# Optimization experiments

Hardware: AMD Instinct MI355X
Metric: run time of the kernel (lower is better)

The kernel has to match this reference:

```python
import jax, jax.numpy as jnp
import numpy as np

EPS = 1e-5

def _act_quant(x):
    # per-token int8 absmax quantization (BitNet b1.58)
    scale = 127.0 / jnp.clip(jnp.max(jnp.abs(x), axis=-1, keepdims=True), EPS)
    return jnp.clip(jnp.round(x * scale), -128.0, 127.0) / scale

def _weight_quant(w):
    # per-tensor ternary quantization: round(w/mean|w|) clipped to {-1,0,1}
    scale = 1.0 / jnp.clip(jnp.mean(jnp.abs(w)), EPS)
    return jnp.clip(jnp.round(w * scale), -1.0, 1.0) / scale

def _ste(x, q):
    # straight-through estimator: forward uses q, backward passes through x
    return x + jax.lax.stop_gradient(q - x)

def bitlinear(x, w):
    xq = _ste(x, _act_quant(x))
    wq = _ste(w, _weight_quant(w))
    return jnp.einsum('btd,hd->bth', xq, wq)

def setup_inputs() -> dict:
    key = jax.random.key(0)
    k1, k2, k3 = jax.random.split(key, 3)
    B, T, D, H = 4, 1024, 2048, 8192
    x = jax.random.normal(k1, (B, T, D), dtype=jnp.float32)
    w1 = jax.random.normal(k2, (H, D), dtype=jnp.float32) * 0.02
    w2 = jax.random.normal(k3, (D, H), dtype=jnp.float32) * 0.02
    return {"x": x, "w1": w1, "w2": w2}

def reference(x, w1, w2):
    h = jax.nn.relu(bitlinear(x, w1))   # [B, T, H]
    out = bitlinear(h, w2)              # [B, T, D]
    return out
```

## Files before the change

### kernel.cpp

```cpp
#include <hip/hip_runtime.h>
#include <hip/hip_bf16.h>

#define EPSF 1e-5f

typedef int v4i __attribute__((ext_vector_type(4)));
typedef short v8s __attribute__((ext_vector_type(8)));

static constexpr int BB = 4, TT = 1024, DD = 2048, HH = 8192;
static constexpr int MROWS = BB * TT;
static constexpr long long WCOUNT = (long long)DD * HH;


__device__ __forceinline__ void async_copy16(const void* g, void* l) {
  __builtin_amdgcn_global_load_lds(
      (const __attribute__((address_space(1))) unsigned int*)g,
      (__attribute__((address_space(3))) unsigned int*)l,
      16, 0, 0);
}

__device__ __forceinline__ int pack4(float a, float b, float c, float d,
                                     float scale, float lo, float hi) {
  int ia = (int)fminf(fmaxf(rintf(a * scale), lo), hi);
  int ib = (int)fminf(fmaxf(rintf(b * scale), lo), hi);
  int ic = (int)fminf(fmaxf(rintf(c * scale), lo), hi);
  int id = (int)fminf(fmaxf(rintf(d * scale), lo), hi);
  return (ia & 0xff) | ((ib & 0xff) << 8) | ((ic & 0xff) << 16) | ((id & 0xff) << 24);
}

__device__ __forceinline__ float abs4(float4 v) {
  return fmaxf(fmaxf(fabsf(v.x), fabsf(v.y)), fmaxf(fabsf(v.z), fabsf(v.w)));
}

__device__ __forceinline__ int blockMaxI256(int v) {
  #pragma unroll
  for (int off = 32; off; off >>= 1) v = max(v, __shfl_down(v, off, 64));
  __shared__ int sm[4];
  int lane = threadIdx.x & 63, wv = threadIdx.x >> 6;
  if (lane == 0) sm[wv] = v;
  __syncthreads();
  return max(max(sm[0], sm[1]), max(sm[2], sm[3]));
}

__device__ __forceinline__ void swizzle_tiles(int& mt, int& nt) {
  int Mt = gridDim.y, Nt = gridDim.x;
  int id = blockIdx.y * Nt + blockIdx.x;
  int c = id & 7, k = id >> 3;
  int pm = (Mt >= Nt) ? 4 : 2;
  int PM = Mt / pm, PN = Nt / (8 / pm);
  int pr = c % pm, pc = c / pm;
  mt = pr * PM + (k % PM);
  nt = pc * PN + (k / PM);
}


__global__ __launch_bounds__(256) void abs_sum_kernel(
    const float* __restrict__ w1, const float* __restrict__ w2,
    float* __restrict__ partials) {
  const int y = blockIdx.y, bid = blockIdx.x, t = threadIdx.x;
  const int lane = t & 63, wv = t >> 6;
  const float4* w4 = (const float4*)(y ? w2 : w1);
  const long long base = (long long)bid * 2048;
  float4 u[8];
  #pragma unroll
  for (int k = 0; k < 8; k++) u[k] = w4[base + t + k * 256];
  float s = 0.f;
  #pragma unroll
  for (int k = 0; k < 8; k++)
    s += fabsf(u[k].x) + fabsf(u[k].y) + fabsf(u[k].z) + fabsf(u[k].w);
  #pragma unroll
  for (int off = 32; off; off >>= 1) s += __shfl_down(s, off, 64);
  __shared__ float sm[4];
  if (lane == 0) sm[wv] = s;
  __syncthreads();
  if (t == 0) partials[y * 2048 + bid] = sm[0] + sm[1] + sm[2] + sm[3];
}


__global__ __launch_bounds__(256) void quant_w_kernel(
    const float* __restrict__ w1, const float* __restrict__ w2,
    const float* __restrict__ partials, float* __restrict__ meanw,
    signed char* __restrict__ q1, signed char* __restrict__ q2) {
  const int y = blockIdx.y, bid = blockIdx.x, t = threadIdx.x;
  const int lane = t & 63, wv = t >> 6;

  double d = 0.0;
  #pragma unroll
  for (int j = 0; j < 8; j++) d += (double)partials[y * 2048 + t + j * 256];
  #pragma unroll
  for (int off = 32; off; off >>= 1) d += __shfl_down(d, off, 64);
  __shared__ double smd[4];
  if (lane == 0) smd[wv] = d;
  __syncthreads();
  double sum = smd[0] + smd[1] + smd[2] + smd[3];
  float mean = fmaxf((float)(sum * (1.0 / (double)WCOUNT)), EPSF);
  if (bid == 0 && t == 0) meanw[y] = mean;
  float sc = 1.0f / mean;

  const float4* w4 = (const float4*)(y ? w2 : w1);
  int* q4 = (int*)(y ? q2 : q1);
  const long long base = (long long)bid * 2048;
  float4 u[8];
  #pragma unroll
  for (int k = 0; k < 8; k++) u[k] = w4[base + t + k * 256];
  #pragma unroll
  for (int k = 0; k < 8; k++)
    q4[base + t + k * 256] = pack4(u[k].x, u[k].y, u[k].z, u[k].w, sc, -1.f, 1.f);
}


__global__ __launch_bounds__(256) void quant_x_kernel(
    const float* __restrict__ x, signed char* __restrict__ xq,
    float* __restrict__ ascale) {
  int lane = threadIdx.x & 63, wv = threadIdx.x >> 6;
  int row = blockIdx.x * 4 + wv;
  const float4* xr = (const float4*)(x + (size_t)row * DD);
  float4 v[8];
  #pragma unroll
  for (int j = 0; j < 8; j++) v[j] = xr[lane + j * 64];
  float m = 0.f;
  #pragma unroll
  for (int j = 0; j < 8; j++) m = fmaxf(m, abs4(v[j]));
  #pragma unroll
  for (int off = 32; off; off >>= 1) m = fmaxf(m, __shfl_down(m, off, 64));
  m = __shfl(m, 0, 64);
  float am = fmaxf(m, EPSF);
  float scale = 127.0f / am;
  int* out = (int*)(xq + (size_t)row * DD);
  #pragma unroll
  for (int j = 0; j < 8; j++)
    out[lane + j * 64] = pack4(v[j].x, v[j].y, v[j].z, v[j].w, scale, -128.f, 127.f);
  if (lane == 0) ascale[row] = am / 127.0f;
}


__global__ __launch_bounds__(256) void quant_h_kernel(
    const short* __restrict__ h, signed char* __restrict__ hq,
    float* __restrict__ a2, const float* __restrict__ a1,
    const float* __restrict__ meanw) {
  int row = blockIdx.x;
  int t = threadIdx.x;
  const v8s* hr = (const v8s*)(h + (size_t)row * HH);
  v8s v[4];
  #pragma unroll
  for (int i = 0; i < 4; i++) v[i] = hr[t + i * 256];
  int mx = 0;
  #pragma unroll
  for (int i = 0; i < 4; i++)
    #pragma unroll
    for (int j = 0; j < 8; j++) mx = max(mx, (int)v[i][j]);
  int bmx = blockMaxI256(mx);
  float f = a1[row] * meanw[0];
  float maxh = (float)bmx * f;
  float am = fmaxf(maxh, EPSF);
  float scale = 127.0f / am;
  int* out = (int*)(hq + (size_t)row * HH);
  #pragma unroll
  for (int i = 0; i < 4; i++) {
    out[(t + i * 256) * 2] =
        pack4((float)v[i][0] * f, (float)v[i][1] * f, (float)v[i][2] * f,
              (float)v[i][3] * f, scale, -128.f, 127.f);
    out[(t + i * 256) * 2 + 1] =
        pack4((float)v[i][4] * f, (float)v[i][5] * f, (float)v[i][6] * f,
              (float)v[i][7] * f, scale, -128.f, 127.f);
  }
  if (t == 0) a2[row] = am / 127.0f;
}


template <int MODE, int BK>
__global__ __launch_bounds__(256) void gemm_i8_kernel(
    const signed char* __restrict__ A, const signed char* __restrict__ B,
    void* __restrict__ Cout, const float* __restrict__ ascale,
    const float* __restrict__ wmean_p, int M, int N, int K) {
  constexpr int CH = BK / 16;
  constexpr int SEGROWS = 1024 / BK;
  constexpr int SPW = BK / 32;
  __shared__ signed char As[128 * BK];
  __shared__ signed char Bs[128 * BK];

  const int t = threadIdx.x;
  const int lane = t & 63, wv = t >> 6;
  const int wm = wv >> 1, wn = wv & 1;
  int mt, nt;
  swizzle_tiles(mt, nt);
  const int m0 = mt * 128, n0 = nt * 128;
  const int q = lane >> 4;

  const signed char* aSrc[SPW];
  const signed char* bSrc[SPW];
  #pragma unroll
  for (int i = 0; i < SPW; i++) {
    int seg = wv * SPW + i;
    int r = seg * SEGROWS + lane / CH;
    int c = (lane % CH) ^ (r & (CH - 1));
    aSrc[i] = A + (size_t)(m0 + r) * K + c * 16;
    bSrc[i] = B + (size_t)(n0 + r) * K + c * 16;
  }

  v4i acc[4][4];
  #pragma unroll
  for (int i = 0; i < 4; i++)
    #pragma unroll
    for (int j = 0; j < 4; j++) {
      v4i z = {0, 0, 0, 0};
      acc[i][j] = z;
    }

  int rowA[4], rowB[4];
  #pragma unroll
  for (int i = 0; i < 4; i++) {
    rowA[i] = wm * 64 + i * 16 + (lane & 15);
    rowB[i] = wn * 64 + i * 16 + (lane & 15);
  }

  for (int k0 = 0; k0 < K; k0 += BK) {
    #pragma unroll
    for (int i = 0; i < SPW; i++) {
      async_copy16(aSrc[i] + k0, &As[(wv * SPW + i) * 1024]);
      async_copy16(bSrc[i] + k0, &Bs[(wv * SPW + i) * 1024]);
    }
    __syncthreads();
    #pragma unroll
    for (int kc = 0; kc < CH / 4; kc++) {
      v4i af[4], bf[4];
      #pragma unroll
      for (int i = 0; i < 4; i++) {
        int ca = (kc * 4 + q) ^ (rowA[i] & (CH - 1));
        af[i] = *(const v4i*)(As + rowA[i] * BK + ca * 16);
        int cb = (kc * 4 + q) ^ (rowB[i] & (CH - 1));
        bf[i] = *(const v4i*)(Bs + rowB[i] * BK + cb * 16);
      }
      #pragma unroll
      for (int i = 0; i < 4; i++)
        #pragma unroll
        for (int j = 0; j < 4; j++)
          acc[i][j] = __builtin_amdgcn_mfma_i32_16x16x64_i8(af[i], bf[j], acc[i][j], 0, 0, 0);
    }
    __syncthreads();
  }

  if constexpr (MODE == 1) {
    short* C = (short*)Cout;
    #pragma unroll
    for (int i = 0; i < 4; i++) {
      int mBase = m0 + wm * 64 + i * 16 + q * 4;
      #pragma unroll
      for (int e = 0; e < 4; e++) {
        #pragma unroll
        for (int j = 0; j < 4; j++) {
          int n = n0 + wn * 64 + j * 16 + (lane & 15);
          int r = acc[i][j][e];
          r = r < 0 ? 0 : (r > 32767 ? 32767 : r);
          C[(size_t)(mBase + e) * N + n] = (short)r;
        }
      }
    }
  } else {
    float* C = (float*)Cout;
    float wmean = wmean_p[0];
    #pragma unroll
    for (int i = 0; i < 4; i++) {
      int mBase = m0 + wm * 64 + i * 16 + q * 4;
      #pragma unroll
      for (int e = 0; e < 4; e++) {
        float f = ascale[mBase + e] * wmean;
        #pragma unroll
        for (int j = 0; j < 4; j++) {
          int n = n0 + wn * 64 + j * 16 + (lane & 15);
          C[(size_t)(mBase + e) * N + n] = (float)acc[i][j][e] * f;
        }
      }
    }
  }
}


extern "C" void kernel_launch(void* const* d_in, const int* in_sizes, int n_in,
                              void* d_out, int out_size, void* d_ws, size_t ws_size,
                              hipStream_t stream) {
  const float* x  = (const float*)d_in[0];
  const float* w1 = (const float*)d_in[1];
  const float* w2 = (const float*)d_in[2];
  float* out = (float*)d_out;

  char* ws = (char*)d_ws;
  float* meanw = (float*)ws;
  float* partials = (float*)(ws + 1024);
  float* a1 = (float*)(ws + 20480);
  float* a2 = (float*)(ws + 40960);
  signed char* w1q = (signed char*)(ws + 65536);
  signed char* w2q = w1q + (size_t)WCOUNT;
  signed char* xq  = w2q + (size_t)WCOUNT;
  signed char* hq  = xq + (size_t)MROWS * DD;
  short* h16 = (short*)(hq + (size_t)MROWS * HH);

  abs_sum_kernel<<<dim3(2048, 2), 256, 0, stream>>>(w1, w2, partials);
  quant_w_kernel<<<dim3(2048, 2), 256, 0, stream>>>(w1, w2, partials, meanw, w1q, w2q);
  quant_x_kernel<<<MROWS / 4, 256, 0, stream>>>(x, xq, a1);
  gemm_i8_kernel<1, 128><<<dim3(HH / 128, MROWS / 128), 256, 0, stream>>>(
      xq, w1q, h16, nullptr, meanw, MROWS, HH, DD);
  quant_h_kernel<<<MROWS, 256, 0, stream>>>(h16, hq, a2, a1, meanw);
  gemm_i8_kernel<0, 256><<<dim3(DD / 128, MROWS / 128), 256, 0, stream>>>(
      hq, w2q, out, a2, &meanw[1], MROWS, DD, HH);
}
```

Baseline: 375.2 us.

## Use 32x32x32 int8 MFMA, fuse x-quant into abs-sum, widen h stores

The GEMM moves from a 4x4 grid of 16x16x64 int8 MFMAs per wave to a 2x2 grid of 32x32x32 MFMAs, which halves the LDS fragment loads per k-step and changes the epilogue row mapping. The x-quantization and weight abs-sum kernels are merged into one launch, saving a kernel launch and letting both run concurrently. quant_h now writes 8 bytes per store instead of two 4-byte stores. The larger MFMA changes the LDS access pattern against the existing swizzle and may cause bank conflicts or different instruction throughput.

```diff
diff --git a/kernel.cpp b/kernel.cpp
--- a/kernel.cpp
+++ b/kernel.cpp
@@ -4,6 +4,7 @@
 #define EPSF 1e-5f
 
 typedef int v4i __attribute__((ext_vector_type(4)));
+typedef int v16i __attribute__((ext_vector_type(16)));
 typedef short v8s __attribute__((ext_vector_type(8)));
 
 static constexpr int BB = 4, TT = 1024, DD = 2048, HH = 8192;
@@ -53,26 +54,50 @@
 }
 
 
-__global__ __launch_bounds__(256) void abs_sum_kernel(
+__global__ __launch_bounds__(256) void prep_kernel(
     const float* __restrict__ w1, const float* __restrict__ w2,
-    float* __restrict__ partials) {
-  const int y = blockIdx.y, bid = blockIdx.x, t = threadIdx.x;
+    const float* __restrict__ x, float* __restrict__ partials,
+    signed char* __restrict__ xq, float* __restrict__ ascale) {
+  __shared__ float sm[4];
+  const int bid = blockIdx.x, t = threadIdx.x;
   const int lane = t & 63, wv = t >> 6;
-  const float4* w4 = (const float4*)(y ? w2 : w1);
-  const long long base = (long long)bid * 2048;
-  float4 u[8];
-  #pragma unroll
-  for (int k = 0; k < 8; k++) u[k] = w4[base + t + k * 256];
-  float s = 0.f;
-  #pragma unroll
-  for (int k = 0; k < 8; k++)
-    s += fabsf(u[k].x) + fabsf(u[k].y) + fabsf(u[k].z) + fabsf(u[k].w);
-  #pragma unroll
-  for (int off = 32; off; off >>= 1) s += __shfl_down(s, off, 64);
-  __shared__ float sm[4];
-  if (lane == 0) sm[wv] = s;
-  __syncthreads();
-  if (t == 0) partials[y * 2048 + bid] = sm[0] + sm[1] + sm[2] + sm[3];
+
+  if (bid < 4096) {
+    const int y = bid >> 11, b = bid & 2047;
+    const float4* w4 = (const float4*)(y ? w2 : w1);
+    const long long base = (long long)b * 2048;
+    float4 u[8];
+    #pragma unroll
+    for (int k = 0; k < 8; k++) u[k] = w4[base + t + k * 256];
+    float s = 0.f;
+    #pragma unroll
+    for (int k = 0; k < 8; k++)
+      s += fabsf(u[k].x) + fabsf(u[k].y) + fabsf(u[k].z) + fabsf(u[k].w);
+    #pragma unroll
+    for (int off = 32; off; off >>= 1) s += __shfl_down(s, off, 64);
+    if (lane == 0) sm[wv] = s;
+    __syncthreads();
+    if (t == 0) partials[y * 2048 + b] = sm[0] + sm[1] + sm[2] + sm[3];
+  } else {
+    int row = (bid - 4096) * 4 + wv;
+    const float4* xr = (const float4*)(x + (size_t)row * DD);
+    float4 v[8];
+    #pragma unroll
+    for (int j = 0; j < 8; j++) v[j] = xr[lane + j * 64];
+    float m = 0.f;
+    #pragma unroll
+    for (int j = 0; j < 8; j++) m = fmaxf(m, abs4(v[j]));
+    #pragma unroll
+    for (int off = 32; off; off >>= 1) m = fmaxf(m, __shfl_down(m, off, 64));
+    m = __shfl(m, 0, 64);
+    float am = fmaxf(m, EPSF);
+    float scale = 127.0f / am;
+    int* out = (int*)(xq + (size_t)row * DD);
+    #pragma unroll
+    for (int j = 0; j < 8; j++)
+      out[lane + j * 64] = pack4(v[j].x, v[j].y, v[j].z, v[j].w, scale, -128.f, 127.f);
+    if (lane == 0) ascale[row] = am / 127.0f;
+  }
 }
 
 
@@ -108,31 +133,6 @@
 }
 
 
-__global__ __launch_bounds__(256) void quant_x_kernel(
-    const float* __restrict__ x, signed char* __restrict__ xq,
-    float* __restrict__ ascale) {
-  int lane = threadIdx.x & 63, wv = threadIdx.x >> 6;
-  int row = blockIdx.x * 4 + wv;
-  const float4* xr = (const float4*)(x + (size_t)row * DD);
-  float4 v[8];
-  #pragma unroll
-  for (int j = 0; j < 8; j++) v[j] = xr[lane + j * 64];
-  float m = 0.f;
-  #pragma unroll
-  for (int j = 0; j < 8; j++) m = fmaxf(m, abs4(v[j]));
-  #pragma unroll
-  for (int off = 32; off; off >>= 1) m = fmaxf(m, __shfl_down(m, off, 64));
-  m = __shfl(m, 0, 64);
-  float am = fmaxf(m, EPSF);
-  float scale = 127.0f / am;
-  int* out = (int*)(xq + (size_t)row * DD);
-  #pragma unroll
-  for (int j = 0; j < 8; j++)
-    out[lane + j * 64] = pack4(v[j].x, v[j].y, v[j].z, v[j].w, scale, -128.f, 127.f);
-  if (lane == 0) ascale[row] = am / 127.0f;
-}
-
-
 __global__ __launch_bounds__(256) void quant_h_kernel(
     const short* __restrict__ h, signed char* __restrict__ hq,
     float* __restrict__ a2, const float* __restrict__ a1,
@@ -153,15 +153,14 @@
   float maxh = (float)bmx * f;
   float am = fmaxf(maxh, EPSF);
   float scale = 127.0f / am;
-  int* out = (int*)(hq + (size_t)row * HH);
+  int2* out = (int2*)(hq + (size_t)row * HH);
   #pragma unroll
   for (int i = 0; i < 4; i++) {
-    out[(t + i * 256) * 2] =
-        pack4((float)v[i][0] * f, (float)v[i][1] * f, (float)v[i][2] * f,
-              (float)v[i][3] * f, scale, -128.f, 127.f);
-    out[(t + i * 256) * 2 + 1] =
-        pack4((float)v[i][4] * f, (float)v[i][5] * f, (float)v[i][6] * f,
-              (float)v[i][7] * f, scale, -128.f, 127.f);
+    int p0 = pack4((float)v[i][0] * f, (float)v[i][1] * f, (float)v[i][2] * f,
+                   (float)v[i][3] * f, scale, -128.f, 127.f);
+    int p1 = pack4((float)v[i][4] * f, (float)v[i][5] * f, (float)v[i][6] * f,
+                   (float)v[i][7] * f, scale, -128.f, 127.f);
+    out[t + i * 256] = int2{p0, p1};
   }
   if (t == 0) a2[row] = am / 127.0f;
 }
@@ -184,7 +183,7 @@
   int mt, nt;
   swizzle_tiles(mt, nt);
   const int m0 = mt * 128, n0 = nt * 128;
-  const int q = lane >> 4;
+  const int hf = lane >> 5;
 
   const signed char* aSrc[SPW];
   const signed char* bSrc[SPW];
@@ -197,20 +196,20 @@
     bSrc[i] = B + (size_t)(n0 + r) * K + c * 16;
   }
 
-  v4i acc[4][4];
-  #pragma unroll
-  for (int i = 0; i < 4; i++)
-    #pragma unroll
-    for (int j = 0; j < 4; j++) {
-      v4i z = {0, 0, 0, 0};
+  v16i acc[2][2];
+  #pragma unroll
+  for (int i = 0; i < 2; i++)
+    #pragma unroll
+    for (int j = 0; j < 2; j++) {
+      v16i z = {0, 0, 0, 0, 0, 0, 0, 0, 0, 0, 0, 0, 0, 0, 0, 0};
       acc[i][j] = z;
     }
 
-  int rowA[4], rowB[4];
-  #pragma unroll
-  for (int i = 0; i < 4; i++) {
-    rowA[i] = wm * 64 + i * 16 + (lane & 15);
-    rowB[i] = wn * 64 + i * 16 + (lane & 15);
+  int rowA[2], rowB[2];
+  #pragma unroll
+  for (int i = 0; i < 2; i++) {
+    rowA[i] = wm * 64 + i * 32 + (lane & 31);
+    rowB[i] = wn * 64 + i * 32 + (lane & 31);
   }
 
   for (int k0 = 0; k0 < K; k0 += BK) {
@@ -221,20 +220,20 @@
     }
     __syncthreads();
     #pragma unroll
-    for (int kc = 0; kc < CH / 4; kc++) {
-      v4i af[4], bf[4];
+    for (int ks = 0; ks < BK / 32; ks++) {
+      v4i af[2], bf[2];
       #pragma unroll
-      for (int i = 0; i < 4; i++) {
-        int ca = (kc * 4 + q) ^ (rowA[i] & (CH - 1));
+      for (int i = 0; i < 2; i++) {
+        int ca = (ks * 2 + hf) ^ (rowA[i] & (CH - 1));
         af[i] = *(const v4i*)(As + rowA[i] * BK + ca * 16);
-        int cb = (kc * 4 + q) ^ (rowB[i] & (CH - 1));
+        int cb = (ks * 2 + hf) ^ (rowB[i] & (CH - 1));
         bf[i] = *(const v4i*)(Bs + rowB[i] * BK + cb * 16);
       }
       #pragma unroll
-      for (int i = 0; i < 4; i++)
+      for (int i = 0; i < 2; i++)
         #pragma unroll
-        for (int j = 0; j < 4; j++)
-          acc[i][j] = __builtin_amdgcn_mfma_i32_16x16x64_i8(af[i], bf[j], acc[i][j], 0, 0, 0);
+        for (int j = 0; j < 2; j++)
+          acc[i][j] = __builtin_amdgcn_mfma_i32_32x32x32_i8(af[i], bf[j], acc[i][j], 0, 0, 0);
     }
     __syncthreads();
   }
@@ -242,16 +241,16 @@
   if constexpr (MODE == 1) {
     short* C = (short*)Cout;
     #pragma unroll
-    for (int i = 0; i < 4; i++) {
-      int mBase = m0 + wm * 64 + i * 16 + q * 4;
+    for (int i = 0; i < 2; i++) {
       #pragma unroll
-      for (int e = 0; e < 4; e++) {
+      for (int e = 0; e < 16; e++) {
+        int m = m0 + wm * 64 + i * 32 + (e & 3) + 8 * (e >> 2) + 4 * hf;
         #pragma unroll
-        for (int j = 0; j < 4; j++) {
-          int n = n0 + wn * 64 + j * 16 + (lane & 15);
+        for (int j = 0; j < 2; j++) {
+          int n = n0 + wn * 64 + j * 32 + (lane & 31);
           int r = acc[i][j][e];
           r = r < 0 ? 0 : (r > 32767 ? 32767 : r);
-          C[(size_t)(mBase + e) * N + n] = (short)r;
+          C[(size_t)m * N + n] = (short)r;
         }
       }
     }
@@ -259,15 +258,15 @@
     float* C = (float*)Cout;
     float wmean = wmean_p[0];
     #pragma unroll
-    for (int i = 0; i < 4; i++) {
-      int mBase = m0 + wm * 64 + i * 16 + q * 4;
+    for (int i = 0; i < 2; i++) {
       #pragma unroll
-      for (int e = 0; e < 4; e++) {
-        float f = ascale[mBase + e] * wmean;
+      for (int e = 0; e < 16; e++) {
+        int m = m0 + wm * 64 + i * 32 + (e & 3) + 8 * (e >> 2) + 4 * hf;
+        float f = ascale[m] * wmean;
         #pragma unroll
-        for (int j = 0; j < 4; j++) {
-          int n = n0 + wn * 64 + j * 16 + (lane & 15);
-          C[(size_t)(mBase + e) * N + n] = (float)acc[i][j][e] * f;
+        for (int j = 0; j < 2; j++) {
+          int n = n0 + wn * 64 + j * 32 + (lane & 31);
+          C[(size_t)m * N + n] = (float)acc[i][j][e] * f;
         }
       }
     }
@@ -294,9 +293,8 @@
   signed char* hq  = xq + (size_t)MROWS * DD;
   short* h16 = (short*)(hq + (size_t)MROWS * HH);
 
-  abs_sum_kernel<<<dim3(2048, 2), 256, 0, stream>>>(w1, w2, partials);
+  prep_kernel<<<5120, 256, 0, stream>>>(w1, w2, x, partials, xq, a1);
   quant_w_kernel<<<dim3(2048, 2), 256, 0, stream>>>(w1, w2, partials, meanw, w1q, w2q);
-  quant_x_kernel<<<MROWS / 4, 256, 0, stream>>>(x, xq, a1);
   gemm_i8_kernel<1, 128><<<dim3(HH / 128, MROWS / 128), 256, 0, stream>>>(
       xq, w1q, h16, nullptr, meanw, MROWS, HH, DD);
   quant_h_kernel<<<MROWS, 256, 0, stream>>>(h16, hq, a2, a1, meanw);
```

Measured after the change: 373.6 us. Within noise of the previous version (-0.4%).
